# Optimization experiments

Hardware: AMD Instinct MI355X
Metric: run time of the kernel (lower is better)

The kernel has to match this reference:

```python
import jax, jax.numpy as jnp
import numpy as np

N, E = 50000, 800000          # nodes, directed edges
DIN, DH, DOUT = 128, 256, 128  # feature dims


def setup_inputs() -> dict:
    key = jax.random.key(0)
    ks = jax.random.split(key, 8)
    glorot = lambda k, fin, fout: jax.random.normal(k, (fin, fout), jnp.float32) * np.float32(1.0 / np.sqrt(fin))
    x = jax.random.normal(ks[0], (N, DIN), jnp.float32)
    edge_index = jax.random.randint(ks[1], (2, E), 0, N, dtype=jnp.int64)
    return {
        "x": x,
        "edge_index": edge_index,
        "W1_l": glorot(ks[2], DIN, DH),   # applied to aggregated neighbors
        "b1": jnp.zeros((DH,), jnp.float32),
        "W1_r": glorot(ks[3], DIN, DH),   # root weight
        "W2_l": glorot(ks[4], DH, DOUT),
        "b2": jnp.zeros((DOUT,), jnp.float32),
        "W2_r": glorot(ks[5], DH, DOUT),
    }


def _sage_conv(x, src, dst, W_l, b, W_r):
    """PyG SAGEConv (mean aggr): lin_l(mean_j x_j) + lin_r(x_i)."""
    n = x.shape[0]
    agg = jax.ops.segment_sum(x[src], dst, num_segments=n)          # [N, D]
    deg = jax.ops.segment_sum(jnp.ones((src.shape[0], 1), x.dtype), dst, num_segments=n)
    agg = agg / jnp.maximum(deg, 1.0)                               # mean over in-neighbors
    return agg @ W_l + b + x @ W_r


def reference(x, edge_index, W1_l, b1, W1_r, W2_l, b2, W2_r):
    src, dst = edge_index[0], edge_index[1]
    h = jax.nn.relu(_sage_conv(x, src, dst, W1_l, b1, W1_r))
    return _sage_conv(h, src, dst, W2_l, b2, W2_r)
```

## Files before the change

kernel.cpp:

```cpp
#include <hip/hip_runtime.h>
#include <hip/hip_bf16.h>
#include <cstdint>


static inline size_t align_up(size_t x, size_t a) { return (x + a - 1) & ~(a - 1); }

using short8 = __attribute__((ext_vector_type(8))) short;
using f32x4  = __attribute__((ext_vector_type(4))) float;

#define BSHIFT 6
#define PB 98

__device__ __forceinline__ float bfpair_lo(unsigned int v) {
  union { unsigned int i; float f; } u; u.i = v << 16; return u.f;
}
__device__ __forceinline__ float bfpair_hi(unsigned int v) {
  union { unsigned int i; float f; } u; u.i = v & 0xffff0000u; return u.f;
}
__device__ __forceinline__ unsigned short f2bf(float f) {
  union { float f; unsigned int i; } u; u.f = f;
  unsigned int r = u.i + 0x7fffu + ((u.i >> 16) & 1u);
  return (unsigned short)(r >> 16);
}

__device__ __forceinline__ void gload_lds16(const void* g, void* l) {
  __builtin_amdgcn_global_load_lds(
      (const __attribute__((address_space(1))) void*)g,
      (__attribute__((address_space(3))) void*)l, 16, 0, 0);
}

__global__ __launch_bounds__(256) void setup_kernel(
    const int* __restrict__ dst, int* __restrict__ blockhist, int E, int chunk,
    const float* __restrict__ x,
    const float* __restrict__ W1l, const float* __restrict__ W1r,
    const float* __restrict__ W2l, const float* __restrict__ W2r,
    __hip_bfloat16* __restrict__ BT1, __hip_bfloat16* __restrict__ BT2,
    __hip_bfloat16* __restrict__ A1, int total4) {
  __shared__ int h[1024];
  const int bb = blockIdx.x;
  const int t = threadIdx.x;
  if (bb < PB) {
    #pragma unroll
    for (int i = t; i < 1024; i += 256) h[i] = 0;
    __syncthreads();
    const int e0 = bb * chunk;
    int e1 = e0 + chunk; if (e1 > E) e1 = E;
    for (int e = e0 + t; e < e1; e += 256) atomicAdd(&h[dst[e] >> BSHIFT], 1);
    __syncthreads();
    #pragma unroll
    for (int i = t; i < 1024; i += 256) blockhist[bb * 1024 + i] = h[i];
    return;
  }
  const int wb = bb - PB;
  if (wb < 512) {
    int idx = (wb & 255) * 256 + t;
    int n = idx >> 8, k = idx & 255;
    if (wb < 256) {
      float v = (k < 128) ? W1l[k * 256 + n] : W1r[(k - 128) * 256 + n];
      BT1[idx] = __float2bfloat16(v);
    } else {
      float v = (n < 128) ? W2l[k * 128 + n] : W2r[k * 128 + (n - 128)];
      BT2[idx] = __float2bfloat16(v);
    }
    return;
  }
  int idx = (wb - 512) * 256 + t;
  if (idx >= total4) return;
  int i = idx >> 5, j4 = (idx & 31) << 2;
  float4 v = *reinterpret_cast<const float4*>(x + (size_t)i * 128 + j4);
  unsigned p0 = ((unsigned)f2bf(v.y) << 16) | f2bf(v.x);
  unsigned p1 = ((unsigned)f2bf(v.w) << 16) | f2bf(v.z);
  *reinterpret_cast<uint2*>(A1 + (size_t)i * 256 + 128 + j4) = make_uint2(p0, p1);
}

__global__ __launch_bounds__(256) void bin2_kernel(const int* __restrict__ src,
                                                   const int* __restrict__ dst,
                                                   const int* __restrict__ blockhist,
                                                   unsigned* __restrict__ stage,
                                                   int* __restrict__ brow,
                                                   int E, int NB, int chunk) {
  __shared__ int tot_lds[1024];
  __shared__ int cur_lds[1024];
  __shared__ int wsum[4];
  const int t = threadIdx.x;
  const int pb = blockIdx.x;

  int run[4] = {0, 0, 0, 0};
  int ownp[4] = {0, 0, 0, 0};
  for (int pb2 = 0; pb2 < PB; ++pb2) {
    #pragma unroll
    for (int j = 0; j < 4; ++j) {
      int v = blockhist[pb2 * 1024 + t + 256 * j];
      if (pb2 == pb) ownp[j] = run[j];
      run[j] += v;
    }
  }
  #pragma unroll
  for (int j = 0; j < 4; ++j) {
    tot_lds[t + 256 * j] = run[j];
    cur_lds[t + 256 * j] = ownp[j];
  }
  __syncthreads();

  int4 v = *reinterpret_cast<const int4*>(&tot_lds[t * 4]);
  int tsum = v.x + v.y + v.z + v.w;
  const int lane = t & 63, w = t >> 6;
  int inc = tsum;
  #pragma unroll
  for (int off = 1; off < 64; off <<= 1) {
    int u = __shfl_up(inc, off, 64);
    if (lane >= off) inc += u;
  }
  if (lane == 63) wsum[w] = inc;
  __syncthreads();
  int woff = 0;
  for (int k = 0; k < w; ++k) woff += wsum[k];
  int e0x = woff + inc - tsum;
  int p0 = e0x, p1 = p0 + v.x, p2 = p1 + v.y, p3 = p2 + v.z;
  cur_lds[t * 4 + 0] += p0;
  cur_lds[t * 4 + 1] += p1;
  cur_lds[t * 4 + 2] += p2;
  cur_lds[t * 4 + 3] += p3;
  if (pb == 0) {
    if (t * 4 + 0 < NB) brow[t * 4 + 0] = p0;
    if (t * 4 + 1 < NB) brow[t * 4 + 1] = p1;
    if (t * 4 + 2 < NB) brow[t * 4 + 2] = p2;
    if (t * 4 + 3 < NB) brow[t * 4 + 3] = p3;
    if (t == 255) brow[NB] = p3 + v.w;
  }
  __syncthreads();

  const int e0 = pb * chunk;
  const int e1 = min(e0 + chunk, E);
  for (int e = e0 + t; e < e1; e += 256) {
    int d = dst[e];
    int p = atomicAdd(&cur_lds[d >> BSHIFT], 1);
    stage[p] = (unsigned)src[e] | ((unsigned)(d & 63) << 16);
  }
}

__global__ __launch_bounds__(256) void scatter2b_kernel(const unsigned* __restrict__ stage,
                                                        const int* __restrict__ brow,
                                                        int* __restrict__ rowptr,
                                                        unsigned short* __restrict__ col,
                                                        int N, int E) {
  __shared__ int dcnt[64];
  __shared__ int dbase[64];
  const int b = blockIdx.x;
  const int t = threadIdx.x;
  const int n0 = b << BSHIFT;
  const int lo = brow[b], hi = brow[b + 1];
  if (t < 64) dcnt[t] = 0;
  __syncthreads();
  for (int e = lo + t; e < hi; e += 256) atomicAdd(&dcnt[stage[e] >> 16], 1);
  __syncthreads();
  if (t < 64) {
    int v = dcnt[t];
    int inc = v;
    #pragma unroll
    for (int off = 1; off < 64; off <<= 1) {
      int u = __shfl_up(inc, off, 64);
      if (t >= off) inc += u;
    }
    int excl = lo + inc - v;
    dbase[t] = excl;
    dcnt[t] = 0;
    if (n0 + t < N) rowptr[n0 + t] = excl;
  }
  if (b == 0 && t == 0) rowptr[N] = E;
  __syncthreads();
  for (int e = lo + t; e < hi; e += 256) {
    unsigned pr = stage[e];
    int d = pr >> 16;
    int p = atomicAdd(&dcnt[d], 1);
    col[dbase[d] + p] = (unsigned short)(pr & 0xffffu);
  }
}


#define AGG_LOAD(TBL, OFFS)                                                    \
  {                                                                            \
    int s = col[eidx];                                                         \
    uint2 vv = *reinterpret_cast<const uint2*>(TBL + (size_t)s * 256 + OFFS + q * 4); \
    a0 += bfpair_lo(vv.x); a1 += bfpair_hi(vv.x);                              \
    a2 += bfpair_lo(vv.y); a3 += bfpair_hi(vv.y);                              \
  }

__global__ __launch_bounds__(64) void agg1_kernel(const int* __restrict__ rowptr,
                                                  const unsigned short* __restrict__ col,
                                                  __hip_bfloat16* __restrict__ A1) {
  const int i = blockIdx.x;
  const int t = threadIdx.x;
  const int half = t >> 5;
  const int q = t & 31;
  const int beg = rowptr[i], end = rowptr[i + 1];
  float a0 = 0.f, a1 = 0.f, a2 = 0.f, a3 = 0.f;
  int e = beg;
  for (; e + 15 < end; e += 16) {
    #pragma unroll
    for (int u = 0; u < 8; ++u) {
      int eidx = e + 2 * u + half;
      AGG_LOAD(A1, 128)
    }
  }
  if (e + 7 < end) {
    #pragma unroll
    for (int u = 0; u < 4; ++u) {
      int eidx = e + 2 * u + half;
      AGG_LOAD(A1, 128)
    }
    e += 8;
  }
  if (e + 3 < end) {
    #pragma unroll
    for (int u = 0; u < 2; ++u) {
      int eidx = e + 2 * u + half;
      AGG_LOAD(A1, 128)
    }
    e += 4;
  }
  if (e + 1 < end) {
    int eidx = e + half;
    AGG_LOAD(A1, 128)
    e += 2;
  }
  if (e < end && half == 0) {
    int eidx = e;
    AGG_LOAD(A1, 128)
  }
  a0 += __shfl_xor(a0, 32, 64);
  a1 += __shfl_xor(a1, 32, 64);
  a2 += __shfl_xor(a2, 32, 64);
  a3 += __shfl_xor(a3, 32, 64);
  const int d = end - beg;
  const float inv = 1.0f / (float)(d > 1 ? d : 1);
  if (half == 0) {
    unsigned p0 = ((unsigned)f2bf(a1 * inv) << 16) | f2bf(a0 * inv);
    unsigned p1 = ((unsigned)f2bf(a3 * inv) << 16) | f2bf(a2 * inv);
    *reinterpret_cast<uint2*>(A1 + (size_t)i * 256 + q * 4) = make_uint2(p0, p1);
  }
}

__global__ __launch_bounds__(64) void agg2_kernel(const __hip_bfloat16* __restrict__ hw2,
                                                  const int* __restrict__ rowptr,
                                                  const unsigned short* __restrict__ col,
                                                  const float* __restrict__ b2,
                                                  float* __restrict__ out) {
  const int i = blockIdx.x;
  const int t = threadIdx.x;
  const int half = t >> 5;
  const int q = t & 31;
  const int beg = rowptr[i], end = rowptr[i + 1];
  float a0 = 0.f, a1 = 0.f, a2 = 0.f, a3 = 0.f;
  int e = beg;
  for (; e + 15 < end; e += 16) {
    #pragma unroll
    for (int u = 0; u < 8; ++u) {
      int eidx = e + 2 * u + half;
      AGG_LOAD(hw2, 0)
    }
  }
  if (e + 7 < end) {
    #pragma unroll
    for (int u = 0; u < 4; ++u) {
      int eidx = e + 2 * u + half;
      AGG_LOAD(hw2, 0)
    }
    e += 8;
  }
  if (e + 3 < end) {
    #pragma unroll
    for (int u = 0; u < 2; ++u) {
      int eidx = e + 2 * u + half;
      AGG_LOAD(hw2, 0)
    }
    e += 4;
  }
  if (e + 1 < end) {
    int eidx = e + half;
    AGG_LOAD(hw2, 0)
    e += 2;
  }
  if (e < end && half == 0) {
    int eidx = e;
    AGG_LOAD(hw2, 0)
  }
  a0 += __shfl_xor(a0, 32, 64);
  a1 += __shfl_xor(a1, 32, 64);
  a2 += __shfl_xor(a2, 32, 64);
  a3 += __shfl_xor(a3, 32, 64);
  const int d = end - beg;
  const float inv = 1.0f / (float)(d > 1 ? d : 1);
  if (half == 0) {
    uint2 sv = *reinterpret_cast<const uint2*>(hw2 + (size_t)i * 256 + 128 + q * 4);
    float4 bb = *reinterpret_cast<const float4*>(b2 + q * 4);
    float4 r;
    r.x = a0 * inv + bfpair_lo(sv.x) + bb.x;
    r.y = a1 * inv + bfpair_hi(sv.x) + bb.y;
    r.z = a2 * inv + bfpair_lo(sv.y) + bb.z;
    r.w = a3 * inv + bfpair_hi(sv.y) + bb.w;
    *reinterpret_cast<float4*>(out + (size_t)i * 128 + q * 4) = r;
  }
}

__global__ __launch_bounds__(256) void gemm_fused_kernel(
    const __hip_bfloat16* __restrict__ A1,
    const __hip_bfloat16* __restrict__ BT1,
    const __hip_bfloat16* __restrict__ BT2,
    const float* __restrict__ b1,
    __hip_bfloat16* __restrict__ hw2,
    int M) {
  __shared__ __hip_bfloat16 As[64 * 32];
  __shared__ __hip_bfloat16 Bs[256 * 32];
  __shared__ __hip_bfloat16 hLds[64 * 256];
  const int t = threadIdx.x;
  const int lane = t & 63;
  const int w = t >> 6;
  const int wc = w * 64;
  const int bm = blockIdx.x * 64;

  const int srow4 = lane >> 2;
  const int sbyte = (lane & 3) * 16;
  const int fr = lane & 15;
  const int fbyte = (lane >> 4) * 16;
  const int kslot = lane >> 4;

  f32x4 acc[4][4];
  #pragma unroll
  for (int i = 0; i < 4; ++i)
    #pragma unroll
    for (int j = 0; j < 4; ++j) acc[i][j] = (f32x4)(0.f);

  for (int k0 = 0; k0 < 256; k0 += 32) {
    {
      int gr = bm + w * 16 + srow4;
      if (gr >= M) gr = M - 1;
      gload_lds16((const char*)A1 + (size_t)gr * 512 + k0 * 2 + sbyte,
                  (char*)As + w * 1024);
    }
    #pragma unroll
    for (int q = 0; q < 4; ++q) {
      const int c = w * 4 + q;
      const int row = c * 16 + srow4;
      gload_lds16((const char*)BT1 + (size_t)row * 512 + k0 * 2 + sbyte,
                  (char*)Bs + c * 1024);
    }
    __syncthreads();
    short8 af[4], bf[4];
    #pragma unroll
    for (int i = 0; i < 4; ++i) {
      af[i] = *reinterpret_cast<const short8*>((const char*)As + (fr + i * 16) * 64 + fbyte);
      bf[i] = *reinterpret_cast<const short8*>((const char*)Bs + (wc + fr + i * 16) * 64 + fbyte);
    }
    #pragma unroll
    for (int i = 0; i < 4; ++i)
      #pragma unroll
      for (int j = 0; j < 4; ++j)
        acc[i][j] = __builtin_amdgcn_mfma_f32_16x16x32_bf16(af[i], bf[j], acc[i][j], 0, 0, 0);
    __syncthreads();
  }

  {
    const int c0 = wc + fr;
    const int r0 = (lane >> 4) * 4;
    float bj[4];
    #pragma unroll
    for (int j = 0; j < 4; ++j) bj[j] = b1[c0 + j * 16];
    #pragma unroll
    for (int i = 0; i < 4; ++i) {
      #pragma unroll
      for (int j = 0; j < 4; ++j) {
        const int c = c0 + j * 16;
        #pragma unroll
        for (int q = 0; q < 4; ++q) {
          const int r = r0 + i * 16 + q;
          float v = fmaxf(acc[i][j][q] + bj[j], 0.f);
          const int byte = r * 512 + (((c >> 3) ^ (r & 7)) << 4) + ((c & 7) << 1);
          *reinterpret_cast<__hip_bfloat16*>((char*)hLds + byte) = __float2bfloat16(v);
        }
      }
    }
  }

  #pragma unroll
  for (int i = 0; i < 4; ++i)
    #pragma unroll
    for (int j = 0; j < 4; ++j) acc[i][j] = (f32x4)(0.f);

  for (int k0 = 0; k0 < 256; k0 += 32) {
    #pragma unroll
    for (int q = 0; q < 4; ++q) {
      const int c = w * 4 + q;
      const int row = c * 16 + srow4;
      gload_lds16((const char*)BT2 + (size_t)row * 512 + k0 * 2 + sbyte,
                  (char*)Bs + c * 1024);
    }
    __syncthreads();
    short8 af[4], bf[4];
    const int ks = (k0 >> 3) + kslot;
    #pragma unroll
    for (int i = 0; i < 4; ++i) {
      const int ra = fr + i * 16;
      af[i] = *reinterpret_cast<const short8*>(
          (const char*)hLds + ra * 512 + ((ks ^ (ra & 7)) << 4));
      bf[i] = *reinterpret_cast<const short8*>((const char*)Bs + (wc + fr + i * 16) * 64 + fbyte);
    }
    #pragma unroll
    for (int i = 0; i < 4; ++i)
      #pragma unroll
      for (int j = 0; j < 4; ++j)
        acc[i][j] = __builtin_amdgcn_mfma_f32_16x16x32_bf16(af[i], bf[j], acc[i][j], 0, 0, 0);
    __syncthreads();
  }

  {
    const int c0 = wc + fr;
    const int r0 = (lane >> 4) * 4;
    #pragma unroll
    for (int i = 0; i < 4; ++i) {
      #pragma unroll
      for (int q = 0; q < 4; ++q) {
        const int r = bm + r0 + i * 16 + q;
        if (r < M) {
          #pragma unroll
          for (int j = 0; j < 4; ++j)
            hw2[(size_t)r * 256 + c0 + j * 16] = __float2bfloat16(acc[i][j][q]);
        }
      }
    }
  }
}


extern "C" void kernel_launch(void* const* d_in, const int* in_sizes, int n_in,
                              void* d_out, int out_size, void* d_ws, size_t ws_size,
                              hipStream_t stream) {
  const float* x    = (const float*)d_in[0];
  const int*   edge = (const int*)d_in[1];
  const float* W1_l = (const float*)d_in[2];
  const float* b1   = (const float*)d_in[3];
  const float* W1_r = (const float*)d_in[4];
  const float* W2_l = (const float*)d_in[5];
  const float* b2   = (const float*)d_in[6];
  const float* W2_r = (const float*)d_in[7];
  float* out = (float*)d_out;

  const int N = in_sizes[0] / 128;
  const int E = in_sizes[1] / 2;
  const int* srcv = edge;
  const int* dstv = edge + E;
  const int NB = (N + (1 << BSHIFT) - 1) >> BSHIFT;

  char* ws = (char*)d_ws;
  size_t off = 0;
  auto alloc = [&](size_t bytes) -> void* {
    void* p = ws + off;
    off += align_up(bytes, 256);
    return p;
  };
  int* rowptr    = (int*)alloc((size_t)(N + 1) * 4);
  int* brow      = (int*)alloc((size_t)(NB + 1) * 4);
  int* blockhist = (int*)alloc((size_t)PB * 1024 * 4);
  unsigned short* col = (unsigned short*)alloc((size_t)E * 2);
  unsigned* stage = (unsigned*)alloc((size_t)E * 4);
  __hip_bfloat16* BT1 = (__hip_bfloat16*)alloc(256 * 256 * 2);
  __hip_bfloat16* BT2 = (__hip_bfloat16*)alloc(256 * 256 * 2);
  __hip_bfloat16* A1  = (__hip_bfloat16*)alloc((size_t)N * 256 * 2);
  __hip_bfloat16* hw2 = (__hip_bfloat16*)alloc((size_t)N * 256 * 2);

  const int chunk = (E + PB - 1) / PB;
  const int conv_blocks = (N * 32 + 255) / 256;
  setup_kernel<<<PB + 512 + conv_blocks, 256, 0, stream>>>(
      dstv, blockhist, E, chunk, x, W1_l, W1_r, W2_l, W2_r, BT1, BT2, A1, N * 32);

  bin2_kernel<<<PB, 256, 0, stream>>>(srcv, dstv, blockhist, stage, brow, E, NB, chunk);
  scatter2b_kernel<<<NB, 256, 0, stream>>>(stage, brow, rowptr, col, N, E);

  agg1_kernel<<<N, 64, 0, stream>>>(rowptr, col, A1);

  gemm_fused_kernel<<<(N + 63) / 64, 256, 0, stream>>>(A1, BT1, BT2, b1, hw2, N);

  agg2_kernel<<<N, 64, 0, stream>>>(hw2, rowptr, col, b2, out);
}
```

Before: 152.0 us.

## Move per-block histogram column scan into a separate parallel kernel

Adds a colscan kernel that computes the exclusive prefix over partition blocks for each of the 1024 bins in parallel using wave shuffles, and also writes the per-bin totals. Before this, every bin2 block serially read all PB rows of the histogram. bin2 now reads only its own offsets row and the totals. PB is raised from 98 to 128 so the binning pass has more blocks, at the cost of one extra kernel launch.

```diff
diff --git a/kernel.cpp b/kernel.cpp
--- a/kernel.cpp
+++ b/kernel.cpp
@@ -9,7 +9,7 @@
 using f32x4  = __attribute__((ext_vector_type(4))) float;
 
 #define BSHIFT 6
-#define PB 98
+#define PB 128
 
 __device__ __forceinline__ float bfpair_lo(unsigned int v) {
   union { unsigned int i; float f; } u; u.i = v << 16; return u.f;
@@ -73,36 +73,40 @@
   *reinterpret_cast<uint2*>(A1 + (size_t)i * 256 + 128 + j4) = make_uint2(p0, p1);
 }
 
+__global__ __launch_bounds__(256) void colscan_kernel(int* __restrict__ blockhist,
+                                                      int* __restrict__ btot) {
+  const int t = threadIdx.x;
+  const int lane = t & 63;
+  const int i = blockIdx.x * 4 + (t >> 6);
+  int v0 = blockhist[lane * 1024 + i];
+  int v1 = (64 + lane < PB) ? blockhist[(64 + lane) * 1024 + i] : 0;
+  int s0 = v0, s1 = v1;
+  #pragma unroll
+  for (int off = 1; off < 64; off <<= 1) {
+    int u0 = __shfl_up(s0, off, 64);
+    int u1 = __shfl_up(s1, off, 64);
+    if (lane >= off) { s0 += u0; s1 += u1; }
+  }
+  const int total0 = __shfl(s0, 63, 64);
+  const int total1 = __shfl(s1, 63, 64);
+  blockhist[lane * 1024 + i] = s0 - v0;
+  if (64 + lane < PB) blockhist[(64 + lane) * 1024 + i] = total0 + s1 - v1;
+  if (lane == 0) btot[i] = total0 + total1;
+}
+
 __global__ __launch_bounds__(256) void bin2_kernel(const int* __restrict__ src,
                                                    const int* __restrict__ dst,
                                                    const int* __restrict__ blockhist,
+                                                   const int* __restrict__ btot,
                                                    unsigned* __restrict__ stage,
                                                    int* __restrict__ brow,
                                                    int E, int NB, int chunk) {
-  __shared__ int tot_lds[1024];
   __shared__ int cur_lds[1024];
   __shared__ int wsum[4];
   const int t = threadIdx.x;
   const int pb = blockIdx.x;
 
-  int run[4] = {0, 0, 0, 0};
-  int ownp[4] = {0, 0, 0, 0};
-  for (int pb2 = 0; pb2 < PB; ++pb2) {
-    #pragma unroll
-    for (int j = 0; j < 4; ++j) {
-      int v = blockhist[pb2 * 1024 + t + 256 * j];
-      if (pb2 == pb) ownp[j] = run[j];
-      run[j] += v;
-    }
-  }
-  #pragma unroll
-  for (int j = 0; j < 4; ++j) {
-    tot_lds[t + 256 * j] = run[j];
-    cur_lds[t + 256 * j] = ownp[j];
-  }
-  __syncthreads();
-
-  int4 v = *reinterpret_cast<const int4*>(&tot_lds[t * 4]);
+  int4 v = *reinterpret_cast<const int4*>(btot + t * 4);
   int tsum = v.x + v.y + v.z + v.w;
   const int lane = t & 63, w = t >> 6;
   int inc = tsum;
@@ -117,10 +121,12 @@
   for (int k = 0; k < w; ++k) woff += wsum[k];
   int e0x = woff + inc - tsum;
   int p0 = e0x, p1 = p0 + v.x, p2 = p1 + v.y, p3 = p2 + v.z;
-  cur_lds[t * 4 + 0] += p0;
-  cur_lds[t * 4 + 1] += p1;
-  cur_lds[t * 4 + 2] += p2;
-  cur_lds[t * 4 + 3] += p3;
+
+  int4 o = *reinterpret_cast<const int4*>(blockhist + pb * 1024 + t * 4);
+  cur_lds[t * 4 + 0] = p0 + o.x;
+  cur_lds[t * 4 + 1] = p1 + o.y;
+  cur_lds[t * 4 + 2] = p2 + o.z;
+  cur_lds[t * 4 + 3] = p3 + o.w;
   if (pb == 0) {
     if (t * 4 + 0 < NB) brow[t * 4 + 0] = p0;
     if (t * 4 + 1 < NB) brow[t * 4 + 1] = p1;
@@ -460,6 +466,7 @@
   };
   int* rowptr    = (int*)alloc((size_t)(N + 1) * 4);
   int* brow      = (int*)alloc((size_t)(NB + 1) * 4);
+  int* btot      = (int*)alloc(1024 * 4);
   int* blockhist = (int*)alloc((size_t)PB * 1024 * 4);
   unsigned short* col = (unsigned short*)alloc((size_t)E * 2);
   unsigned* stage = (unsigned*)alloc((size_t)E * 4);
@@ -473,7 +480,8 @@
   setup_kernel<<<PB + 512 + conv_blocks, 256, 0, stream>>>(
       dstv, blockhist, E, chunk, x, W1_l, W1_r, W2_l, W2_r, BT1, BT2, A1, N * 32);
 
-  bin2_kernel<<<PB, 256, 0, stream>>>(srcv, dstv, blockhist, stage, brow, E, NB, chunk);
+  colscan_kernel<<<256, 256, 0, stream>>>(blockhist, btot);
+  bin2_kernel<<<PB, 256, 0, stream>>>(srcv, dstv, blockhist, btot, stage, brow, E, NB, chunk);
   scatter2b_kernel<<<NB, 256, 0, stream>>>(stage, brow, rowptr, col, N, E);
 
   agg1_kernel<<<N, 64, 0, stream>>>(rowptr, col, A1);
```

Measured after the change: 133.7 us (median of 2 runs). 12.0% less time.
